# Kernel tuning notes

Hardware: AMD Instinct MI355X
Metric: run time of the kernel (lower is better)

## Reference

```python
import jax, jax.numpy as jnp
import numpy as np

B, T, C, H = 2, 2048, 1024, 16
D = C // H  # d_head = 64


def setup_inputs() -> dict:
    key = jax.random.key(0)
    k1, k2, k3 = jax.random.split(key, 3)
    x = jax.random.normal(k1, (B, T, C), dtype=jnp.float32)
    # torch Linear weights stored pre-transposed as [in, out] so we apply x @ W
    w_qkv = jax.random.normal(k2, (C, 3 * C), dtype=jnp.float32) * (C ** -0.5)
    w_out = jax.random.normal(k3, (C, C), dtype=jnp.float32) * (C ** -0.5)
    charge_w = jnp.array([0.0, 3.0, 6.0], dtype=jnp.float32)  # CHARGES init
    # causal mask, broadcast over batch and heads; mask==0 positions are blocked
    mask = jnp.tril(jnp.ones((1, 1, T, T), dtype=jnp.int32))
    return {"x": x, "mask": mask, "w_qkv": w_qkv, "w_out": w_out, "charge_w": charge_w}


def reference(x, mask, w_qkv, w_out, charge_w):
    B, T, C = x.shape
    H = 16
    D = C // H
    qkv = (x @ w_qkv).reshape(B, T, 3, H, D)
    q, k, v = qkv[:, :, 0], qkv[:, :, 1], qkv[:, :, 2]  # each [B,T,H,D]
    scale = D ** -0.5
    attn = jnp.einsum("bqhd,bkhd->bhqk", q, k) * scale  # [B,H,T,T]
    charge_bias = jnp.mod(jnp.sum(charge_w), 9.0) * 0.001  # scalar bias
    attn = attn + charge_bias
    attn = jnp.where(mask == 0, jnp.float32(-1e9), attn)
    attn = jax.nn.softmax(attn, axis=-1)  # dropout is identity in eval mode
    out = jnp.einsum("bhqk,bkhd->bqhd", attn, v).reshape(B, T, C)
    return out @ w_out
```

## Files before the change

### kernel.cpp

```cpp
#include <hip/hip_runtime.h>
#include <stdint.h>


typedef __attribute__((ext_vector_type(4))) float f32x4;
typedef __attribute__((ext_vector_type(16))) float f32x16;
typedef __attribute__((ext_vector_type(8))) __bf16 bf16x8;
typedef __attribute__((ext_vector_type(8))) unsigned short ushort8;
typedef __attribute__((ext_vector_type(4))) unsigned short ushort4v;
typedef __attribute__((ext_vector_type(4))) unsigned int uint4v;

#define DEV __device__ __forceinline__

DEV unsigned short f32_to_bf16(float f) {
    union { float f; unsigned int u; } cv; cv.f = f;
    unsigned int u = cv.u;
    return (unsigned short)((u + 0x7FFFu + ((u >> 16) & 1u)) >> 16);
}

DEV float bf16_to_f32(unsigned short u) {
    union { unsigned int i; float f; } cv; cv.i = ((unsigned int)u) << 16;
    return cv.f;
}

DEV bf16x8 load_bf16x8(const unsigned short* p) {
    ushort8 v = *(const ushort8*)p;
    return __builtin_bit_cast(bf16x8, v);
}

DEV unsigned cvt_pk_bf16(float lo, float hi) {
    unsigned r;
    asm("v_cvt_pk_bf16_f32 %0, %1, %2" : "=v"(r) : "v"(lo), "v"(hi));
    return r;
}

DEV void gload_lds16(const void* g, void* l) {
    __builtin_amdgcn_global_load_lds(
        (const __attribute__((address_space(1))) unsigned int*)g,
        (__attribute__((address_space(3))) unsigned int*)l, 16, 0, 0);
}

DEV f32x16 vzero16() {
    f32x16 v;
#pragma unroll
    for (int i = 0; i < 16; ++i) v[i] = 0.f;
    return v;
}

DEV float tmax32(const f32x16& a, const f32x16& b) {
    float m[16];
#pragma unroll
    for (int i = 0; i < 16; ++i) m[i] = fmaxf(a[i], b[i]);
#pragma unroll
    for (int st = 8; st > 0; st >>= 1)
#pragma unroll
        for (int i = 0; i < 8; ++i) if (i < st) m[i] = fmaxf(m[i], m[i + st]);
    return m[0];
}
DEV float tsum32(const f32x16& a, const f32x16& b) {
    float m[16];
#pragma unroll
    for (int i = 0; i < 16; ++i) m[i] = a[i] + b[i];
#pragma unroll
    for (int st = 8; st > 0; st >>= 1)
#pragma unroll
        for (int i = 0; i < 8; ++i) if (i < st) m[i] = m[i] + m[i + st];
    return m[0];
}

__device__ __constant__ unsigned char qQ[32]  = { 6, 5,14,14,14,13, 9, 9, 4,13,13,12,12, 8, 8,15,15,15,15,12,11,11,11,10, 7, 7, 3,10,10, 2, 1, 0};
__device__ __constant__ unsigned char tsQ[32] = { 0, 0, 0,10,20, 0, 0,10, 0,10,19, 0, 9, 0, 9, 0, 8,16,24,18, 0, 8,16, 0, 0, 8, 0, 8,15, 0, 0, 0};
__device__ __constant__ unsigned char teQ[32] = {14,12,10,20,30,10,10,20,10,19,28, 9,18, 9,18, 8,16,24,32,26, 8,16,24, 8, 8,16, 8,15,22, 6, 4, 2};
__device__ __constant__ unsigned char mlQ[32] = {255,255, 4, 5, 6, 7,19,20,255, 8, 9,10,11,21,22, 0, 1, 2, 3,12,13,14,15,16,23,24,255,17,18,255,255,255};
__device__ __constant__ unsigned char obQ[32] = {255,255,255, 3, 4,255,255,13,255, 5, 6,255, 7,255,14,255, 0, 1, 2, 8,255, 9,10,255,255,15,255,11,12,255,255,255};
__device__ __constant__ unsigned char ncs[9]  = {4,3,3,3,3,3,2,2,2};
__device__ __constant__ unsigned char mlbs[9] = {0,4,7,10,13,16,19,21,23};
__device__ __constant__ unsigned char obbs[9] = {0,3,5,7,9,11,13,14,15};

__global__ void cvt_kernel(const float* __restrict__ in, unsigned short* __restrict__ out, int n) {
    int i = (blockIdx.x * blockDim.x + threadIdx.x) * 8;
    if (i >= n) return;
    f32x4 a = *(const f32x4*)(in + i);
    f32x4 b = *(const f32x4*)(in + i + 4);
    ushort8 o;
    o[0] = f32_to_bf16(a[0]); o[1] = f32_to_bf16(a[1]);
    o[2] = f32_to_bf16(a[2]); o[3] = f32_to_bf16(a[3]);
    o[4] = f32_to_bf16(b[0]); o[5] = f32_to_bf16(b[1]);
    o[6] = f32_to_bf16(b[2]); o[7] = f32_to_bf16(b[3]);
    *(ushort8*)(out + i) = o;
}

__global__ __launch_bounds__(256) void tcvt_kernel(const float* __restrict__ in,
                                                   unsigned short* __restrict__ out,
                                                   int R, int Cn) {
    __shared__ float tl[32][33];
    const int tx = threadIdx.x & 31, ty = threadIdx.x >> 5;
    const int c0 = blockIdx.x * 32, r0 = blockIdx.y * 32;
#pragma unroll
    for (int rr = 0; rr < 4; ++rr) {
        int r = ty + rr * 8;
        tl[r][tx] = in[(size_t)(r0 + r) * Cn + c0 + tx];
    }
    __syncthreads();
#pragma unroll
    for (int rr = 0; rr < 4; ++rr) {
        int cc = ty + rr * 8;
        out[(size_t)(c0 + cc) * R + r0 + tx] = f32_to_bf16(tl[tx][cc]);
    }
}

template<bool OUT_BF16, bool SCALE_Q>
__global__ __launch_bounds__(256) void gemm_kernel(
    const unsigned short* __restrict__ A,
    const unsigned short* __restrict__ Bt,
    void* __restrict__ C, int K, int ldc)
{
    __shared__ __align__(16) unsigned short As[3][4096];
    __shared__ __align__(16) unsigned short Bs[3][4096];

    const int tid = threadIdx.x;
    const int lane = tid & 63;
    const int w = tid >> 6;
    const int wr = w >> 1, wc = w & 1;
    const int g = lane >> 4, ci = lane & 15;
    const int bx = blockIdx.x, by = blockIdx.y;
    const int soff = w * 1024 + lane * 16;
    const int srow = soff >> 6;
    const int scch = (soff >> 4) & 3;

#define GSTAGE(buf, k0_) do { \
    _Pragma("unroll") for (int i_ = 0; i_ < 2; ++i_) { \
        int row_ = srow + i_ * 64; \
        gload_lds16(A  + (size_t)(by * 128 + row_) * K + (k0_) + scch * 8, \
                    (char*)As[buf] + i_ * 4096 + w * 1024); \
        gload_lds16(Bt + (size_t)(bx * 128 + row_) * K + (k0_) + scch * 8, \
                    (char*)Bs[buf] + i_ * 4096 + w * 1024); } } while (0)

    f32x4 acc[4][4];
#pragma unroll
    for (int i = 0; i < 4; ++i)
#pragma unroll
        for (int j = 0; j < 4; ++j) acc[i][j] = f32x4{0.f, 0.f, 0.f, 0.f};

    const int nk = K >> 5;
    GSTAGE(0, 0);
    GSTAGE(1, 32);
    asm volatile("s_waitcnt vmcnt(4)" ::: "memory");
    __builtin_amdgcn_sched_barrier(0);
    __builtin_amdgcn_s_barrier();
    __builtin_amdgcn_sched_barrier(0);

    for (int kt = 0; kt < nk; ++kt) {
        const int cur = kt % 3;
        if (kt + 2 < nk) GSTAGE((kt + 2) % 3, (kt + 2) << 5);

        bf16x8 af[4], bfr[4];
#pragma unroll
        for (int mf = 0; mf < 4; ++mf) af[mf]  = load_bf16x8(&As[cur][(wr * 64 + mf * 16 + ci) * 32 + g * 8]);
#pragma unroll
        for (int nf = 0; nf < 4; ++nf) bfr[nf] = load_bf16x8(&Bs[cur][(wc * 64 + nf * 16 + ci) * 32 + g * 8]);
        __builtin_amdgcn_s_setprio(1);
#pragma unroll
        for (int mf = 0; mf < 4; ++mf)
#pragma unroll
            for (int nf = 0; nf < 4; ++nf)
                acc[mf][nf] = __builtin_amdgcn_mfma_f32_16x16x32_bf16(af[mf], bfr[nf], acc[mf][nf], 0, 0, 0);
        __builtin_amdgcn_s_setprio(0);

        if (kt + 2 < nk) asm volatile("s_waitcnt vmcnt(4) lgkmcnt(0)" ::: "memory");
        else             asm volatile("s_waitcnt vmcnt(0) lgkmcnt(0)" ::: "memory");
        __builtin_amdgcn_sched_barrier(0);
        __builtin_amdgcn_s_barrier();
        __builtin_amdgcn_sched_barrier(0);
    }
#undef GSTAGE

#pragma unroll
    for (int mf = 0; mf < 4; ++mf)
#pragma unroll
        for (int nf = 0; nf < 4; ++nf)
#pragma unroll
            for (int r = 0; r < 4; ++r) {
                int row = by * 128 + wr * 64 + mf * 16 + g * 4 + r;
                int col = bx * 128 + wc * 64 + nf * 16 + ci;
                float v = acc[mf][nf][r];
                if (SCALE_Q && col < 1024) v *= 0.1803368801f;
                if (OUT_BF16)
                    ((unsigned short*)C)[(size_t)row * ldc + col] = f32_to_bf16(v);
                else
                    ((float*)C)[(size_t)row * ldc + col] = v;
            }
}

__global__ __launch_bounds__(256) void attn7_kernel(const unsigned short* __restrict__ qkv,
                                                    unsigned short* __restrict__ attn,
                                                    unsigned short* __restrict__ Obuf,
                                                    float* __restrict__ mlbuf) {
    constexpr int T = 2048, HD3 = 3072, Cc = 1024;
    __shared__ __align__(16) unsigned short Ks[3][4096];
    __shared__ __align__(16) unsigned short Vt[2][4096];

    const int tid = threadIdx.x;
    const int lane = tid & 63;
    const int w = tid >> 6;
    const int l31 = lane & 31;
    const int hi = lane >> 5;

    const int bx = blockIdx.x;
    const int j = bx >> 5;
    const int bh = bx & 31;
    const int q = qQ[j];
    const int ts = tsQ[j], te = teQ[j];
    const int h = bh & 15;
    const int b = bh >> 4;
    const int q0w = q * 128 + w * 32;
    const int qrow = q0w + l31;
    const size_t base = (size_t)b * T * HD3;
    const int ntc = te - ts;

    bf16x8 qf[4];
#pragma unroll
    for (int t = 0; t < 4; ++t)
        qf[t] = load_bf16x8(qkv + base + (size_t)qrow * HD3 + h * 64 + t * 16 + hi * 8);

    f32x16 acc0 = vzero16(), acc1 = vzero16();
    float m = -3e38f, l = 0.f;

    ushort8 vA0, vA1, vB0, vB1;
#define LOADV(tile, r0, r1) do { int kv0_ = (tile) * 64; \
    int rr0_ = tid >> 3, cc0_ = tid & 7; \
    r0 = *(const ushort8*)(qkv + base + (size_t)(kv0_ + rr0_) * HD3 + 2 * Cc + h * 64 + cc0_ * 8); \
    int c1_ = 256 + tid; int rr1_ = c1_ >> 3, cc1_ = c1_ & 7; \
    r1 = *(const ushort8*)(qkv + base + (size_t)(kv0_ + rr1_) * HD3 + 2 * Cc + h * 64 + cc1_ * 8); } while (0)

#define DMAK(tile, kb) do { int kv0_ = (tile) * 64; \
    _Pragma("unroll") for (int i_ = 0; i_ < 2; ++i_) { \
        int off_ = i_ * 4096 + w * 1024 + lane * 16; \
        int row_ = off_ >> 7; \
        int csw_ = ((lane & 7) * 8) ^ ((row_ & 7) * 8); \
        gload_lds16(qkv + base + (size_t)(kv0_ + row_) * HD3 + Cc + h * 64 + csw_, \
                    (void*)(((char*)&Ks[kb][0]) + i_ * 4096 + w * 1024)); } } while (0)

#define WRITEV(vb, r0, r1) do { \
    _Pragma("unroll") for (int i_ = 0; i_ < 2; ++i_) { \
        int c_ = i_ * 256 + tid; int row_ = c_ >> 3, cc_ = c_ & 7; \
        ushort8 v_ = i_ ? r1 : r0; \
        _Pragma("unroll") for (int j_ = 0; j_ < 8; ++j_) { \
            int d_ = cc_ * 8 + j_; \
            int sw_ = ((d_ ^ (d_ >> 3)) & 7) * 8; \
            Vt[vb][d_ * 64 + (row_ ^ sw_)] = v_[j_]; } } } while (0)

    LOADV(ts, vA0, vA1);
    DMAK(ts, 0);
    asm volatile("s_waitcnt vmcnt(0)" ::: "memory");
    __builtin_amdgcn_sched_barrier(0);
    WRITEV(0, vA0, vA1);
    LOADV(ts + 1, vB0, vB1);
    DMAK(ts + 1, 1);
    asm volatile("s_waitcnt lgkmcnt(0)" ::: "memory");
    __builtin_amdgcn_sched_barrier(0);
    __builtin_amdgcn_s_barrier();
    __builtin_amdgcn_sched_barrier(0);

    for (int tt = 0; tt < ntc; ++tt) {
        const int t = ts + tt;
        const int kv0 = t * 64;
        const int kcur = tt % 3;
        const int vcur = tt & 1;
        const bool act = (kv0 <= q0w + 31);
        const bool pre2 = (tt + 2) < ntc;

        if (tt + 1 < ntc) {
            if (tt & 1) WRITEV(vcur ^ 1, vA0, vA1); else WRITEV(vcur ^ 1, vB0, vB1);
        }
        if (pre2) {
            if (tt & 1) LOADV(t + 2, vB0, vB1); else LOADV(t + 2, vA0, vA1);
            DMAK(t + 2, (tt + 2) % 3);
        }

        if (act) {
            f32x16 s0 = vzero16(), s1 = vzero16();
            bf16x8 pf[4];
            const bool st1_ok = (kv0 + 32 <= q0w + 31);
            __builtin_amdgcn_s_setprio(1);
#pragma unroll
            for (int tf = 0; tf < 4; ++tf) {
                int row = l31;
                int idx = kcur * 4096 + row * 64 + ((tf * 16 + hi * 8) ^ ((row & 7) * 8));
                s0 = __builtin_amdgcn_mfma_f32_32x32x16_bf16(load_bf16x8(&Ks[0][idx]), qf[tf], s0, 0, 0, 0);
            }
            if (st1_ok) {
#pragma unroll
                for (int tf = 0; tf < 4; ++tf) {
                    int row = 32 + l31;
                    int idx = kcur * 4096 + row * 64 + ((tf * 16 + hi * 8) ^ ((row & 7) * 8));
                    s1 = __builtin_amdgcn_mfma_f32_32x32x16_bf16(load_bf16x8(&Ks[0][idx]), qf[tf], s1, 0, 0, 0);
                }
            }
            __builtin_amdgcn_s_setprio(0);
            const bool needmask = (kv0 + 63 > q0w);
            if (needmask) {
#pragma unroll
                for (int G = 0; G < 4; ++G)
#pragma unroll
                    for (int rr = 0; rr < 4; ++rr) {
                        int kvb = kv0 + 8 * G + 4 * hi + rr;
                        s0[G * 4 + rr] = (kvb      <= qrow) ? s0[G * 4 + rr] : -3e38f;
                        s1[G * 4 + rr] = (kvb + 32 <= qrow) ? s1[G * 4 + rr] : -3e38f;
                    }
            }
            float pmax = tmax32(s0, s1);
            pmax = fmaxf(pmax, __shfl_xor(pmax, 32));
            if (!__all(pmax - m <= 11.5f)) {
                float mnew = fmaxf(m, pmax);
                float alpha = exp2f(m - mnew);
                m = mnew;
                l *= alpha;
#pragma unroll
                for (int i = 0; i < 16; ++i) { acc0[i] *= alpha; acc1[i] *= alpha; }
            }
#pragma unroll
            for (int i = 0; i < 16; ++i) {
                s0[i] = exp2f(s0[i] - m);
                s1[i] = exp2f(s1[i] - m);
            }

            unsigned pk0[4][2], pk1[4][2];
#pragma unroll
            for (int G = 0; G < 4; ++G) {
                pk0[G][0] = cvt_pk_bf16(s0[G * 4 + 0], s0[G * 4 + 1]);
                pk0[G][1] = cvt_pk_bf16(s0[G * 4 + 2], s0[G * 4 + 3]);
                pk1[G][0] = cvt_pk_bf16(s1[G * 4 + 0], s1[G * 4 + 1]);
                pk1[G][1] = cvt_pk_bf16(s1[G * 4 + 2], s1[G * 4 + 3]);
            }
#pragma unroll
            for (int tf = 0; tf < 4; ++tf) {
                const int kb = tf & 1;
                unsigned sA0, sA1, sB0, sB1;
                if (tf < 2) { sA0 = pk0[2 * kb][0]; sA1 = pk0[2 * kb][1]; sB0 = pk0[2 * kb + 1][0]; sB1 = pk0[2 * kb + 1][1]; }
                else        { sA0 = pk1[2 * kb][0]; sA1 = pk1[2 * kb][1]; sB0 = pk1[2 * kb + 1][0]; sB1 = pk1[2 * kb + 1][1]; }
                unsigned sd0 = hi ? sA0 : sB0, sd1 = hi ? sA1 : sB1;
                unsigned rc0 = (unsigned)__shfl_xor((int)sd0, 32);
                unsigned rc1 = (unsigned)__shfl_xor((int)sd1, 32);
                uint4v u;
                u[0] = hi ? rc0 : sA0;  u[1] = hi ? rc1 : sA1;
                u[2] = hi ? sB0 : rc0;  u[3] = hi ? sB1 : rc1;
                pf[tf] = __builtin_bit_cast(bf16x8, u);
            }

            __builtin_amdgcn_s_setprio(1);
#pragma unroll
            for (int tf = 0; tf < 4; ++tf) {
                {
                    int d = l31, sw = ((d ^ (d >> 3)) & 7) * 8;
                    bf16x8 vf = load_bf16x8(&Vt[vcur][d * 64 + ((tf * 16 + hi * 8) ^ sw)]);
                    acc0 = __builtin_amdgcn_mfma_f32_32x32x16_bf16(vf, pf[tf], acc0, 0, 0, 0);
                }
                {
                    int d = 32 + l31, sw = ((d ^ (d >> 3)) & 7) * 8;
                    bf16x8 vf = load_bf16x8(&Vt[vcur][d * 64 + ((tf * 16 + hi * 8) ^ sw)]);
                    acc1 = __builtin_amdgcn_mfma_f32_32x32x16_bf16(vf, pf[tf], acc1, 0, 0, 0);
                }
            }
            __builtin_amdgcn_s_setprio(0);

            float rsum = tsum32(s0, s1);
            l += rsum + __shfl_xor(rsum, 32);
        }

        if (pre2) asm volatile("s_waitcnt vmcnt(4) lgkmcnt(0)" ::: "memory");
        else      asm volatile("s_waitcnt vmcnt(0) lgkmcnt(0)" ::: "memory");
        __builtin_amdgcn_sched_barrier(0);
        __builtin_amdgcn_s_barrier();
        __builtin_amdgcn_sched_barrier(0);
    }

    const int mlq = mlQ[j], obq = obQ[j];
    if (mlq == 255) {
        const float invl = 1.0f / l;
        const size_t ob = (size_t)b * T * Cc + (size_t)qrow * Cc + h * 64;
#pragma unroll
        for (int G = 0; G < 4; ++G) {
            ushort4v o0, o1;
#pragma unroll
            for (int rr = 0; rr < 4; ++rr) {
                o0[rr] = f32_to_bf16(acc0[G * 4 + rr] * invl);
                o1[rr] = f32_to_bf16(acc1[G * 4 + rr] * invl);
            }
            int d0 = 8 * G + 4 * hi;
            *(ushort4v*)(attn + ob + d0) = o0;
            *(ushort4v*)(attn + ob + 32 + d0) = o1;
        }
    } else {
        const int qlocal = w * 32 + l31;
        unsigned short* op = (obq == 255)
            ? (attn + (size_t)b * T * Cc + (size_t)qrow * Cc + h * 64)
            : (Obuf + (size_t)(bh * 16 + obq) * 8192 + qlocal * 64);
#pragma unroll
        for (int G = 0; G < 4; ++G) {
            ushort4v o0, o1;
#pragma unroll
            for (int rr = 0; rr < 4; ++rr) {
                o0[rr] = f32_to_bf16(acc0[G * 4 + rr]);
                o1[rr] = f32_to_bf16(acc1[G * 4 + rr]);
            }
            int d0 = 8 * G + 4 * hi;
            *(ushort4v*)(op + d0) = o0;
            *(ushort4v*)(op + 32 + d0) = o1;
        }
        if (hi == 0) {
            float* mp = mlbuf + (size_t)(bh * 25 + mlq) * 256 + qlocal * 2;
            mp[0] = m; mp[1] = l;
        }
    }
#undef LOADV
#undef DMAK
#undef WRITEV
}

__global__ __launch_bounds__(256) void combine3_kernel(const unsigned short* __restrict__ Obuf,
                                                       const float* __restrict__ mlbuf,
                                                       unsigned short* __restrict__ attn) {
    constexpr int T = 2048, Cc = 1024;
    const int ss = blockIdx.x;
    const int bh = ss / 9, s = ss - bh * 9;
    const int q = 15 - s;
    const int nc = ncs[s], mlb = mlbs[s], obb = obbs[s];
    const int b = bh >> 4, h = bh & 15;
    const int tid = threadIdx.x;
    const int qlocal = tid >> 1, dh = (tid & 1) * 32;

    float mv[4], lv[4];
#pragma unroll
    for (int c = 0; c < 4; ++c) {
        mv[c] = -3e38f; lv[c] = 0.f;
        if (c < nc) {
            const float* mp = mlbuf + (size_t)(bh * 25 + mlb + c) * 256 + qlocal * 2;
            mv[c] = mp[0]; lv[c] = mp[1];
        }
    }
    float M = fmaxf(fmaxf(mv[0], mv[1]), fmaxf(mv[2], mv[3]));
    float fc[4];
    float denom = 0.f;
#pragma unroll
    for (int c = 0; c < 4; ++c) {
        fc[c] = (c < nc) ? exp2f(mv[c] - M) : 0.f;
        denom += fc[c] * lv[c];
    }
    const float inv = 1.f / denom;
#pragma unroll
    for (int c = 0; c < 4; ++c) fc[c] *= inv;

    unsigned short* po = attn + (size_t)b * T * Cc + (size_t)(q * 128 + qlocal) * Cc + h * 64 + dh;
#pragma unroll
    for (int i = 0; i < 4; ++i) {
        float acc[8] = {0.f, 0.f, 0.f, 0.f, 0.f, 0.f, 0.f, 0.f};
#pragma unroll
        for (int c = 0; c < 4; ++c) {
            if (c < nc) {
                const unsigned short* pc = (c == 0)
                    ? po
                    : (Obuf + (size_t)(bh * 16 + obb + c - 1) * 8192 + qlocal * 64 + dh);
                ushort8 a = *(const ushort8*)(pc + i * 8);
#pragma unroll
                for (int k = 0; k < 8; ++k) acc[k] += fc[c] * bf16_to_f32(a[k]);
            }
        }
        ushort8 o;
#pragma unroll
        for (int k = 0; k < 8; ++k) o[k] = f32_to_bf16(acc[k]);
        *(ushort8*)(po + i * 8) = o;
    }
}

extern "C" void kernel_launch(void* const* d_in, const int* in_sizes, int n_in,
                              void* d_out, int out_size, void* d_ws, size_t ws_size,
                              hipStream_t stream) {
    const float* x     = (const float*)d_in[0];
    const float* w_qkv = (const float*)d_in[2];
    const float* w_out = (const float*)d_in[3];
    float* out = (float*)d_out;

    unsigned short* xb     = (unsigned short*)d_ws;
    unsigned short* wqkvT  = xb + 4194304;
    unsigned short* woutT  = wqkvT + 3145728;
    unsigned short* qkv    = woutT + 1048576;
    unsigned short* attn   = qkv + 12582912;
    unsigned short* Obuf   = xb;
    float*          mlbuf  = (float*)wqkvT;

    cvt_kernel<<<2048, 256, 0, stream>>>(x, xb, 4194304);
    tcvt_kernel<<<dim3(96, 32), 256, 0, stream>>>(w_qkv, wqkvT, 1024, 3072);
    tcvt_kernel<<<dim3(32, 32), 256, 0, stream>>>(w_out, woutT, 1024, 1024);

    gemm_kernel<true, true><<<dim3(24, 32), 256, 0, stream>>>(xb, wqkvT, (void*)qkv, 1024, 3072);

    attn7_kernel<<<1024, 256, 0, stream>>>(qkv, attn, Obuf, mlbuf);
    combine3_kernel<<<288, 256, 0, stream>>>(Obuf, mlbuf, attn);

    gemm_kernel<false, false><<<dim3(8, 32), 256, 0, stream>>>(attn, woutT, (void*)out, 1024, 1024);
}
```

Baseline: 138.4 us.

## Use 256-query attention blocks with 8 waves and rebalanced split-KV schedule

The attention kernel now runs 512-thread blocks covering 256 query rows (8 waves of 32 rows) instead of 128, so each K/V tile loaded into shared memory is reused by twice as many waves. Each thread now issues one V load and one K DMA per tile. The static split-KV work tables, Obuf/mlbuf layouts and the combine kernel are rebuilt for the 256-row granularity, giving 512 attention blocks and 160 combine blocks. Fewer, larger blocks may hurt load balance and occupancy across the causal triangle.

```diff
diff --git a/kernel.cpp b/kernel.cpp
--- a/kernel.cpp
+++ b/kernel.cpp
@@ -67,14 +67,15 @@
     return m[0];
 }
 
-__device__ __constant__ unsigned char qQ[32]  = { 6, 5,14,14,14,13, 9, 9, 4,13,13,12,12, 8, 8,15,15,15,15,12,11,11,11,10, 7, 7, 3,10,10, 2, 1, 0};
-__device__ __constant__ unsigned char tsQ[32] = { 0, 0, 0,10,20, 0, 0,10, 0,10,19, 0, 9, 0, 9, 0, 8,16,24,18, 0, 8,16, 0, 0, 8, 0, 8,15, 0, 0, 0};
-__device__ __constant__ unsigned char teQ[32] = {14,12,10,20,30,10,10,20,10,19,28, 9,18, 9,18, 8,16,24,32,26, 8,16,24, 8, 8,16, 8,15,22, 6, 4, 2};
-__device__ __constant__ unsigned char mlQ[32] = {255,255, 4, 5, 6, 7,19,20,255, 8, 9,10,11,21,22, 0, 1, 2, 3,12,13,14,15,16,23,24,255,17,18,255,255,255};
-__device__ __constant__ unsigned char obQ[32] = {255,255,255, 3, 4,255,255,13,255, 5, 6,255, 7,255,14,255, 0, 1, 2, 8,255, 9,10,255,255,15,255,11,12,255,255,255};
-__device__ __constant__ unsigned char ncs[9]  = {4,3,3,3,3,3,2,2,2};
-__device__ __constant__ unsigned char mlbs[9] = {0,4,7,10,13,16,19,21,23};
-__device__ __constant__ unsigned char obbs[9] = {0,3,5,7,9,11,13,14,15};
+__device__ __constant__ unsigned char qS[16]  = {5, 5, 2, 6, 4, 4, 6, 6, 7, 7, 7, 7, 3, 3, 1, 0};
+__device__ __constant__ unsigned char tsS[16] = {0,12, 0, 0, 0,10,10,19, 0, 8,16,24, 0, 8, 0, 0};
+__device__ __constant__ unsigned char teS[16] = {12,24,12,10,10,20,19,28, 8,16,24,32, 8,16, 8, 4};
+__device__ __constant__ unsigned char mlS[16] = {7, 8,255, 4, 9,10, 5, 6, 0, 1, 2, 3,11,12,255,255};
+__device__ __constant__ unsigned char obS[16] = {255,5,255,255,255,6, 3, 4,255, 0, 1, 2,255, 7,255,255};
+__device__ __constant__ unsigned char qs4[5]   = {7,6,5,4,3};
+__device__ __constant__ unsigned char ncs4[5]  = {4,3,2,2,2};
+__device__ __constant__ unsigned char mlbs4[5] = {0,4,7,9,11};
+__device__ __constant__ unsigned char obbs4[5] = {0,3,5,6,7};
 
 __global__ void cvt_kernel(const float* __restrict__ in, unsigned short* __restrict__ out, int n) {
     int i = (blockIdx.x * blockDim.x + threadIdx.x) * 8;
@@ -191,10 +192,10 @@
             }
 }
 
-__global__ __launch_bounds__(256) void attn7_kernel(const unsigned short* __restrict__ qkv,
-                                                    unsigned short* __restrict__ attn,
-                                                    unsigned short* __restrict__ Obuf,
-                                                    float* __restrict__ mlbuf) {
+__global__ __launch_bounds__(512, 4) void attn8_kernel(const unsigned short* __restrict__ qkv,
+                                                       unsigned short* __restrict__ attn,
+                                                       unsigned short* __restrict__ Obuf,
+                                                       float* __restrict__ mlbuf) {
     constexpr int T = 2048, HD3 = 3072, Cc = 1024;
     __shared__ __align__(16) unsigned short Ks[3][4096];
     __shared__ __align__(16) unsigned short Vt[2][4096];
@@ -208,11 +209,11 @@
     const int bx = blockIdx.x;
     const int j = bx >> 5;
     const int bh = bx & 31;
-    const int q = qQ[j];
-    const int ts = tsQ[j], te = teQ[j];
+    const int q = qS[j];
+    const int ts = tsS[j], te = teS[j];
     const int h = bh & 15;
     const int b = bh >> 4;
-    const int q0w = q * 128 + w * 32;
+    const int q0w = q * 256 + w * 32;
     const int qrow = q0w + l31;
     const size_t base = (size_t)b * T * HD3;
     const int ntc = te - ts;
@@ -225,36 +226,30 @@
     f32x16 acc0 = vzero16(), acc1 = vzero16();
     float m = -3e38f, l = 0.f;
 
-    ushort8 vA0, vA1, vB0, vB1;
-#define LOADV(tile, r0, r1) do { int kv0_ = (tile) * 64; \
+    ushort8 vA0, vB0;
+#define LOADV(tile, r0) do { int kv0_ = (tile) * 64; \
     int rr0_ = tid >> 3, cc0_ = tid & 7; \
-    r0 = *(const ushort8*)(qkv + base + (size_t)(kv0_ + rr0_) * HD3 + 2 * Cc + h * 64 + cc0_ * 8); \
-    int c1_ = 256 + tid; int rr1_ = c1_ >> 3, cc1_ = c1_ & 7; \
-    r1 = *(const ushort8*)(qkv + base + (size_t)(kv0_ + rr1_) * HD3 + 2 * Cc + h * 64 + cc1_ * 8); } while (0)
+    r0 = *(const ushort8*)(qkv + base + (size_t)(kv0_ + rr0_) * HD3 + 2 * Cc + h * 64 + cc0_ * 8); } while (0)
 
 #define DMAK(tile, kb) do { int kv0_ = (tile) * 64; \
-    _Pragma("unroll") for (int i_ = 0; i_ < 2; ++i_) { \
-        int off_ = i_ * 4096 + w * 1024 + lane * 16; \
-        int row_ = off_ >> 7; \
-        int csw_ = ((lane & 7) * 8) ^ ((row_ & 7) * 8); \
-        gload_lds16(qkv + base + (size_t)(kv0_ + row_) * HD3 + Cc + h * 64 + csw_, \
-                    (void*)(((char*)&Ks[kb][0]) + i_ * 4096 + w * 1024)); } } while (0)
-
-#define WRITEV(vb, r0, r1) do { \
-    _Pragma("unroll") for (int i_ = 0; i_ < 2; ++i_) { \
-        int c_ = i_ * 256 + tid; int row_ = c_ >> 3, cc_ = c_ & 7; \
-        ushort8 v_ = i_ ? r1 : r0; \
-        _Pragma("unroll") for (int j_ = 0; j_ < 8; ++j_) { \
-            int d_ = cc_ * 8 + j_; \
-            int sw_ = ((d_ ^ (d_ >> 3)) & 7) * 8; \
-            Vt[vb][d_ * 64 + (row_ ^ sw_)] = v_[j_]; } } } while (0)
-
-    LOADV(ts, vA0, vA1);
+    int row_ = tid >> 3; \
+    int csw_ = (((tid & 7) * 8) ^ ((row_ & 7) * 8)); \
+    gload_lds16(qkv + base + (size_t)(kv0_ + row_) * HD3 + Cc + h * 64 + csw_, \
+                (void*)(((char*)&Ks[kb][0]) + tid * 16)); } while (0)
+
+#define WRITEV(vb, r0) do { \
+    int row_ = tid >> 3, cc_ = tid & 7; \
+    _Pragma("unroll") for (int j_ = 0; j_ < 8; ++j_) { \
+        int d_ = cc_ * 8 + j_; \
+        int sw_ = ((d_ ^ (d_ >> 3)) & 7) * 8; \
+        Vt[vb][d_ * 64 + (row_ ^ sw_)] = r0[j_]; } } while (0)
+
+    LOADV(ts, vA0);
     DMAK(ts, 0);
     asm volatile("s_waitcnt vmcnt(0)" ::: "memory");
     __builtin_amdgcn_sched_barrier(0);
-    WRITEV(0, vA0, vA1);
-    LOADV(ts + 1, vB0, vB1);
+    WRITEV(0, vA0);
+    LOADV(ts + 1, vB0);
     DMAK(ts + 1, 1);
     asm volatile("s_waitcnt lgkmcnt(0)" ::: "memory");
     __builtin_amdgcn_sched_barrier(0);
@@ -270,10 +265,10 @@
         const bool pre2 = (tt + 2) < ntc;
 
         if (tt + 1 < ntc) {
-            if (tt & 1) WRITEV(vcur ^ 1, vA0, vA1); else WRITEV(vcur ^ 1, vB0, vB1);
+            if (tt & 1) WRITEV(vcur ^ 1, vA0); else WRITEV(vcur ^ 1, vB0);
         }
         if (pre2) {
-            if (tt & 1) LOADV(t + 2, vB0, vB1); else LOADV(t + 2, vA0, vA1);
+            if (tt & 1) LOADV(t + 2, vB0); else LOADV(t + 2, vA0);
             DMAK(t + 2, (tt + 2) % 3);
         }
 
@@ -367,14 +362,15 @@
             l += rsum + __shfl_xor(rsum, 32);
         }
 
-        if (pre2) asm volatile("s_waitcnt vmcnt(4) lgkmcnt(0)" ::: "memory");
+        if (pre2) asm volatile("s_waitcnt vmcnt(2) lgkmcnt(0)" ::: "memory");
         else      asm volatile("s_waitcnt vmcnt(0) lgkmcnt(0)" ::: "memory");
         __builtin_amdgcn_sched_barrier(0);
         __builtin_amdgcn_s_barrier();
         __builtin_amdgcn_sched_barrier(0);
     }
 
-    const int mlq = mlQ[j], obq = obQ[j];
+    const int mlq = mlS[j], obq = obS[j];
+    const int qlocal = w * 32 + l31;
     if (mlq == 255) {
         const float invl = 1.0f / l;
         const size_t ob = (size_t)b * T * Cc + (size_t)qrow * Cc + h * 64;
@@ -391,10 +387,9 @@
             *(ushort4v*)(attn + ob + 32 + d0) = o1;
         }
     } else {
-        const int qlocal = w * 32 + l31;
         unsigned short* op = (obq == 255)
             ? (attn + (size_t)b * T * Cc + (size_t)qrow * Cc + h * 64)
-            : (Obuf + (size_t)(bh * 16 + obq) * 8192 + qlocal * 64);
+            : (Obuf + (size_t)(bh * 8 + obq) * 16384 + qlocal * 64);
 #pragma unroll
         for (int G = 0; G < 4; ++G) {
             ushort4v o0, o1;
@@ -408,7 +403,7 @@
             *(ushort4v*)(op + 32 + d0) = o1;
         }
         if (hi == 0) {
-            float* mp = mlbuf + (size_t)(bh * 25 + mlq) * 256 + qlocal * 2;
+            float* mp = mlbuf + (size_t)(bh * 13 + mlq) * 512 + qlocal * 2;
             mp[0] = m; mp[1] = l;
         }
     }
@@ -417,24 +412,23 @@
 #undef WRITEV
 }
 
-__global__ __launch_bounds__(256) void combine3_kernel(const unsigned short* __restrict__ Obuf,
+__global__ __launch_bounds__(256) void combine4_kernel(const unsigned short* __restrict__ Obuf,
                                                        const float* __restrict__ mlbuf,
                                                        unsigned short* __restrict__ attn) {
     constexpr int T = 2048, Cc = 1024;
     const int ss = blockIdx.x;
-    const int bh = ss / 9, s = ss - bh * 9;
-    const int q = 15 - s;
-    const int nc = ncs[s], mlb = mlbs[s], obb = obbs[s];
+    const int bh = ss / 5, s = ss - bh * 5;
+    const int q = qs4[s];
+    const int nc = ncs4[s], mlb = mlbs4[s], obb = obbs4[s];
     const int b = bh >> 4, h = bh & 15;
-    const int tid = threadIdx.x;
-    const int qlocal = tid >> 1, dh = (tid & 1) * 32;
+    const int qlocal = threadIdx.x;
 
     float mv[4], lv[4];
 #pragma unroll
     for (int c = 0; c < 4; ++c) {
         mv[c] = -3e38f; lv[c] = 0.f;
         if (c < nc) {
-            const float* mp = mlbuf + (size_t)(bh * 25 + mlb + c) * 256 + qlocal * 2;
+            const float* mp = mlbuf + (size_t)(bh * 13 + mlb + c) * 512 + qlocal * 2;
             mv[c] = mp[0]; lv[c] = mp[1];
         }
     }
@@ -450,16 +444,16 @@
 #pragma unroll
     for (int c = 0; c < 4; ++c) fc[c] *= inv;
 
-    unsigned short* po = attn + (size_t)b * T * Cc + (size_t)(q * 128 + qlocal) * Cc + h * 64 + dh;
-#pragma unroll
-    for (int i = 0; i < 4; ++i) {
+    unsigned short* po = attn + (size_t)b * T * Cc + (size_t)(q * 256 + qlocal) * Cc + h * 64;
+#pragma unroll
+    for (int i = 0; i < 8; ++i) {
         float acc[8] = {0.f, 0.f, 0.f, 0.f, 0.f, 0.f, 0.f, 0.f};
 #pragma unroll
         for (int c = 0; c < 4; ++c) {
             if (c < nc) {
                 const unsigned short* pc = (c == 0)
                     ? po
-                    : (Obuf + (size_t)(bh * 16 + obb + c - 1) * 8192 + qlocal * 64 + dh);
+                    : (Obuf + (size_t)(bh * 8 + obb + c - 1) * 16384 + qlocal * 64);
                 ushort8 a = *(const ushort8*)(pc + i * 8);
 #pragma unroll
                 for (int k = 0; k < 8; ++k) acc[k] += fc[c] * bf16_to_f32(a[k]);
@@ -494,8 +488,8 @@
 
     gemm_kernel<true, true><<<dim3(24, 32), 256, 0, stream>>>(xb, wqkvT, (void*)qkv, 1024, 3072);
 
-    attn7_kernel<<<1024, 256, 0, stream>>>(qkv, attn, Obuf, mlbuf);
-    combine3_kernel<<<288, 256, 0, stream>>>(Obuf, mlbuf, attn);
+    attn8_kernel<<<512, 512, 0, stream>>>(qkv, attn, Obuf, mlbuf);
+    combine4_kernel<<<160, 256, 0, stream>>>(Obuf, mlbuf, attn);
 
     gemm_kernel<false, false><<<dim3(8, 32), 256, 0, stream>>>(attn, woutT, (void*)out, 1024, 1024);
 }
```

After: 150.0 us. 8.3% more time.
